# Optimization experiments

Hardware: AMD Instinct MI355X
Metric: run time of the kernel (lower is better)

Reference implementation:

```python
import jax, jax.numpy as jnp
import numpy as np

B, S, HID, H, DK = 2, 2048, 1024, 16, 64
SCALE = DK ** -0.5
NEG = -1000000000.0


def setup_inputs() -> dict:
    key = jax.random.key(0)
    ks = jax.random.split(key, 14)
    std = HID ** -0.5
    return {
        "q": jax.random.normal(ks[0], (B, S, HID), jnp.float32),
        "k": jax.random.normal(ks[1], (B, S, HID), jnp.float32),
        "v": jax.random.normal(ks[2], (B, S, HID), jnp.float32),
        "attn_bias": jax.random.normal(ks[3], (B, H, S, S), jnp.float32),
        "mask": jax.random.randint(ks[4], (B, S), 0, 2, jnp.int32),
        "Wq": jax.random.normal(ks[5], (HID, H * DK), jnp.float32) * std,
        "bq": jnp.zeros((H * DK,), jnp.float32),
        "Wk": jax.random.normal(ks[6], (HID, H * DK), jnp.float32) * std,
        "bk": jnp.zeros((H * DK,), jnp.float32),
        "Wv": jax.random.normal(ks[7], (HID, H * DK), jnp.float32) * std,
        "bv": jnp.zeros((H * DK,), jnp.float32),
        "Wo": jax.random.normal(ks[8], (H * DK, H * DK), jnp.float32) * std,
        "bo": jnp.zeros((H * DK,), jnp.float32),
    }


def reference(q, k, v, attn_bias, mask, Wq, bq, Wk, bk, Wv, bv, Wo, bo):
    Bq = q.shape[0]
    # projections -> [B, H, S, DK]
    qh = (q @ Wq + bq).reshape(Bq, -1, H, DK).transpose(0, 2, 1, 3) * SCALE
    kh = (k @ Wk + bk).reshape(Bq, -1, H, DK).transpose(0, 2, 1, 3)
    vh = (v @ Wv + bv).reshape(Bq, -1, H, DK).transpose(0, 2, 1, 3)
    # scores [B, H, Sq, Sk]
    scores = jnp.einsum("bhqd,bhkd->bhqk", qh, kh)
    k_mask = mask[:, None, None, :]  # [B,1,1,Sk]
    scores = jnp.where(k_mask == 0, NEG, scores)
    scores = scores + attn_bias
    attn = jax.nn.softmax(scores, axis=-1)  # dropout rate 0.0 -> identity
    x = jnp.einsum("bhqk,bhkd->bhqd", attn, vh)
    x = x * mask[:, None, :, None].astype(x.dtype)  # zero masked query rows
    x = x.transpose(0, 2, 1, 3).reshape(Bq, -1, H * DK)
    return x @ Wo + bo
```

## Files before the change

### kernel.cpp

```cpp
#include <hip/hip_runtime.h>


typedef __bf16 bf16x8 __attribute__((ext_vector_type(8)));
typedef float f32x4 __attribute__((ext_vector_type(4)));
typedef unsigned short u16x8 __attribute__((ext_vector_type(8)));

#define NEGV (-1000000000.0f)

typedef __attribute__((address_space(3))) unsigned int lds_u32;
typedef const __attribute__((address_space(1))) unsigned int glb_u32;

static __device__ __forceinline__ void async16(const void* g, void* l) {
  __builtin_amdgcn_global_load_lds((glb_u32*)g, (lds_u32*)l, 16, 0, 0);
}

static __device__ __forceinline__ unsigned short f2b(float f) {
  unsigned int u = __float_as_uint(f);
  return (unsigned short)((u + 0x7FFFu + ((u >> 16) & 1u)) >> 16);
}

static __device__ __forceinline__ bf16x8 ld8(const unsigned short* p) {
  return __builtin_bit_cast(bf16x8, *(const u16x8*)p);
}

__global__ __launch_bounds__(256) void k_wtrans(const float* __restrict__ W0, const float* __restrict__ W1,
                                                const float* __restrict__ W2, const float* __restrict__ W3,
                                                unsigned short* __restrict__ T0, unsigned short* __restrict__ T1,
                                                unsigned short* __restrict__ T2, unsigned short* __restrict__ T3) {
  const float* W = (blockIdx.z == 0) ? W0 : (blockIdx.z == 1) ? W1 : (blockIdx.z == 2) ? W2 : W3;
  unsigned short* Wt = (blockIdx.z == 0) ? T0 : (blockIdx.z == 1) ? T1 : (blockIdx.z == 2) ? T2 : T3;
  __shared__ float tile[32][33];
  int k0 = blockIdx.x * 32, n0 = blockIdx.y * 32;
  int tx = threadIdx.x, ty = threadIdx.y;
  #pragma unroll
  for (int i = 0; i < 32; i += 8)
    tile[ty + i][tx] = W[(size_t)(k0 + ty + i) * 1024 + n0 + tx];
  __syncthreads();
  #pragma unroll
  for (int i = 0; i < 32; i += 8)
    Wt[(size_t)(n0 + ty + i) * 1024 + k0 + tx] = f2b(tile[tx][ty + i]);
}

__global__ __launch_bounds__(256) void k_gemm(const float* __restrict__ Af,
                                              const unsigned short* __restrict__ Ab,
                                              const unsigned short* __restrict__ Bt,
                                              const float* __restrict__ bias,
                                              unsigned short* __restrict__ outb,
                                              float* __restrict__ outf, int mode) {
  __shared__ __align__(16) unsigned short smem[128 * 136];
  unsigned short* As = smem;
  unsigned short* Bs = smem + 128 * 64;
  int t = threadIdx.x;
  int wave = t >> 6, lane = t & 63;
  int r16 = lane & 15, quad = lane >> 4, quad8 = quad * 8;
  int wm = (wave >> 1) * 64, wn = (wave & 1) * 64;
  int n0 = blockIdx.x * 128, m0 = blockIdx.y * 128;
  f32x4 acc[4][4] = {};

  for (int k0 = 0; k0 < 1024; k0 += 64) {
    __syncthreads();
    if (mode != 3) {
      int g = t & 7;
      #pragma unroll
      for (int rr = 0; rr < 4; rr++) {
        int row = (t >> 3) + rr * 32;
        const float* p = Af + (size_t)(m0 + row) * 1024 + k0 + g * 8;
        float4 f0 = *(const float4*)p;
        float4 f1 = *(const float4*)(p + 4);
        u16x8 h;
        h[0] = f2b(f0.x); h[1] = f2b(f0.y); h[2] = f2b(f0.z); h[3] = f2b(f0.w);
        h[4] = f2b(f1.x); h[5] = f2b(f1.y); h[6] = f2b(f1.z); h[7] = f2b(f1.w);
        *(u16x8*)&As[row * 64 + ((g ^ (row & 7))) * 8] = h;
      }
    } else {
      #pragma unroll
      for (int i = 0; i < 4; i++) {
        int row = wave * 32 + i * 8 + (lane >> 3);
        const unsigned short* g = Ab + (size_t)(m0 + row) * 1024 + k0 + (((lane & 7) ^ (row & 7))) * 8;
        async16(g, &As[(wave * 32 + i * 8) * 64]);
      }
    }
    #pragma unroll
    for (int i = 0; i < 4; i++) {
      int row = wave * 32 + i * 8 + (lane >> 3);
      const unsigned short* g = Bt + (size_t)(n0 + row) * 1024 + k0 + (((lane & 7) ^ (row & 7))) * 8;
      async16(g, &Bs[(wave * 32 + i * 8) * 64]);
    }
    __syncthreads();
    #pragma unroll
    for (int kk2 = 0; kk2 < 2; kk2++) {
      bf16x8 av[4], bv[4];
      int gq = quad + kk2 * 4;
      #pragma unroll
      for (int mt = 0; mt < 4; mt++) {
        int lm = wm + mt * 16 + r16;
        av[mt] = ld8(&As[lm * 64 + (gq ^ (lm & 7)) * 8]);
      }
      #pragma unroll
      for (int nt = 0; nt < 4; nt++) {
        int ln = wn + nt * 16 + r16;
        bv[nt] = ld8(&Bs[ln * 64 + (gq ^ (ln & 7)) * 8]);
      }
      #pragma unroll
      for (int mt = 0; mt < 4; mt++)
        #pragma unroll
        for (int nt = 0; nt < 4; nt++)
          acc[mt][nt] = __builtin_amdgcn_mfma_f32_16x16x32_bf16(av[mt], bv[nt], acc[mt][nt], 0, 0, 0);
    }
  }

  if (mode == 3) {
    #pragma unroll
    for (int nt = 0; nt < 4; nt++) {
      int gn = n0 + wn + nt * 16 + r16;
      float bv = bias[gn];
      #pragma unroll
      for (int mt = 0; mt < 4; mt++)
        #pragma unroll
        for (int r = 0; r < 4; r++) {
          int gm = m0 + wm + mt * 16 + quad * 4 + r;
          outf[(size_t)gm * 1024 + gn] = acc[mt][nt][r] + bv;
        }
    }
    return;
  }

  __syncthreads();
  float scale = (mode == 0) ? 0.125f : 1.0f;
  #pragma unroll
  for (int nt = 0; nt < 4; nt++) {
    int ln = wn + nt * 16 + r16;
    float bv = bias[n0 + ln];
    #pragma unroll
    for (int mt = 0; mt < 4; mt++)
      #pragma unroll
      for (int r = 0; r < 4; r++) {
        int lm = wm + mt * 16 + quad * 4 + r;
        unsigned short hv = f2b((acc[mt][nt][r] + bv) * scale);
        if (mode == 2) smem[ln * 136 + lm] = hv;
        else           smem[lm * 136 + ln] = hv;
      }
  }
  __syncthreads();
  int rrow = t >> 1, half = t & 1;
  const unsigned short* src = smem + rrow * 136 + half * 64;
  if (mode == 2) {
    int b = m0 >> 11, s0 = m0 & 2047;
    int gn = n0 + rrow, h = gn >> 6, d = gn & 63;
    unsigned short* dst = outb + ((size_t)(b * 16 + h) * 64 + d) * 2048 + s0 + half * 64;
    #pragma unroll
    for (int j = 0; j < 8; j++) *(int4*)(dst + j * 8) = *(const int4*)(src + j * 8);
  } else {
    int gm = m0 + rrow, b = gm >> 11, s = gm & 2047;
    int h = (n0 + half * 64) >> 6;
    unsigned short* dst = outb + ((size_t)(b * 16 + h) * 2048 + s) * 64;
    #pragma unroll
    for (int j = 0; j < 8; j++) *(int4*)(dst + j * 8) = *(const int4*)(src + j * 8);
  }
}

__global__ __launch_bounds__(256) void k_attn(const unsigned short* __restrict__ qh,
                                              const unsigned short* __restrict__ kh,
                                              const unsigned short* __restrict__ vt,
                                              const float* __restrict__ bias,
                                              const int* __restrict__ mask,
                                              unsigned short* __restrict__ xb) {
  __shared__ __align__(16) unsigned short Ks[64 * 72];
  __shared__ __align__(16) unsigned short Vs[64 * 72];
  __shared__ __align__(16) unsigned short Ps[64 * 72];
  __shared__ float kmb[64];
  int t = threadIdx.x;
  int wave = t >> 6, lane = t & 63;
  int r16 = lane & 15, quad = lane >> 4, quad8 = quad * 8;
  int w16 = wave * 16;
  int q0 = blockIdx.x * 64;
  int bh = blockIdx.y;
  int b = bh >> 4, h = bh & 15;
  const unsigned short* kbase = kh + (size_t)bh * 2048 * 64;
  const unsigned short* vbase = vt + (size_t)bh * 64 * 2048;
  const float* bbase = bias + (size_t)bh * 2048 * 2048 + (size_t)q0 * 2048;

  bf16x8 qf[2];
  {
    const unsigned short* qrow = qh + (size_t)bh * 2048 * 64 + (size_t)(q0 + w16 + r16) * 64;
    qf[0] = ld8(qrow + quad8);
    qf[1] = ld8(qrow + 32 + quad8);
  }
  const u16x8 onesu = {0x3F80, 0x3F80, 0x3F80, 0x3F80, 0x3F80, 0x3F80, 0x3F80, 0x3F80};
  const bf16x8 ones = __builtin_bit_cast(bf16x8, onesu);

  f32x4 o[4] = {};
  f32x4 accl = {};
  float mrow[4] = {-1e38f, -1e38f, -1e38f, -1e38f};

  for (int k0 = 0; k0 < 2048; k0 += 64) {
    __syncthreads();
    {
      int row = t >> 2, c = (t & 3) * 16;
      *(int4*)&Ks[row * 72 + c]     = *(const int4*)(kbase + (size_t)(k0 + row) * 64 + c);
      *(int4*)&Ks[row * 72 + c + 8] = *(const int4*)(kbase + (size_t)(k0 + row) * 64 + c + 8);
      *(int4*)&Vs[row * 72 + c]     = *(const int4*)(vbase + (size_t)row * 2048 + k0 + c);
      *(int4*)&Vs[row * 72 + c + 8] = *(const int4*)(vbase + (size_t)row * 2048 + k0 + c + 8);
    }
    if (t < 64) kmb[t] = (mask[b * 2048 + k0 + t] == 0) ? 1.0f : 0.0f;
    __syncthreads();

    f32x4 sc[4] = {};
    #pragma unroll
    for (int kk2 = 0; kk2 < 2; kk2++) {
      #pragma unroll
      for (int nt = 0; nt < 4; nt++) {
        bf16x8 bb = ld8(&Ks[(nt * 16 + r16) * 72 + kk2 * 32 + quad8]);
        sc[nt] = __builtin_amdgcn_mfma_f32_16x16x32_bf16(qf[kk2], bb, sc[nt], 0, 0, 0);
      }
    }
    #pragma unroll
    for (int nt = 0; nt < 4; nt++) {
      float km = kmb[nt * 16 + r16];
      #pragma unroll
      for (int r = 0; r < 4; r++) {
        float bval = bbase[(size_t)(w16 + quad * 4 + r) * 2048 + k0 + nt * 16 + r16];
        sc[nt][r] = ((km > 0.5f) ? NEGV : sc[nt][r]) + bval;
      }
    }
    float arow[4];
    #pragma unroll
    for (int r = 0; r < 4; r++) {
      float mx = fmaxf(fmaxf(sc[0][r], sc[1][r]), fmaxf(sc[2][r], sc[3][r]));
      #pragma unroll
      for (int off = 1; off < 16; off <<= 1) mx = fmaxf(mx, __shfl_xor(mx, off));
      float mn = fmaxf(mrow[r], mx);
      arow[r] = __expf(mrow[r] - mn);
      mrow[r] = mn;
      #pragma unroll
      for (int nt = 0; nt < 4; nt++) sc[nt][r] = __expf(sc[nt][r] - mn);
    }
    #pragma unroll
    for (int nt = 0; nt < 4; nt++)
      #pragma unroll
      for (int r = 0; r < 4; r++)
        Ps[(w16 + quad * 4 + r) * 72 + nt * 16 + r16] = f2b(sc[nt][r]);
    #pragma unroll
    for (int r = 0; r < 4; r++) {
      accl[r] *= arow[r];
      #pragma unroll
      for (int nt = 0; nt < 4; nt++) o[nt][r] *= arow[r];
    }
    #pragma unroll
    for (int kk2 = 0; kk2 < 2; kk2++) {
      bf16x8 a = ld8(&Ps[(w16 + r16) * 72 + kk2 * 32 + quad8]);
      accl = __builtin_amdgcn_mfma_f32_16x16x32_bf16(a, ones, accl, 0, 0, 0);
      #pragma unroll
      for (int nt = 0; nt < 4; nt++) {
        bf16x8 bb = ld8(&Vs[(nt * 16 + r16) * 72 + kk2 * 32 + quad8]);
        o[nt] = __builtin_amdgcn_mfma_f32_16x16x32_bf16(a, bb, o[nt], 0, 0, 0);
      }
    }
  }

  float inv[4];
  #pragma unroll
  for (int r = 0; r < 4; r++) {
    int gq = q0 + w16 + quad * 4 + r;
    float qm = (mask[b * 2048 + gq] != 0) ? 1.0f : 0.0f;
    inv[r] = qm / accl[r];
  }
  #pragma unroll
  for (int nt = 0; nt < 4; nt++)
    #pragma unroll
    for (int r = 0; r < 4; r++) {
      int gq = q0 + w16 + quad * 4 + r;
      xb[(size_t)(b * 2048 + gq) * 1024 + h * 64 + nt * 16 + r16] = f2b(o[nt][r] * inv[r]);
    }
}

extern "C" void kernel_launch(void* const* d_in, const int* in_sizes, int n_in,
                              void* d_out, int out_size, void* d_ws, size_t ws_size,
                              hipStream_t stream) {
  const float* q = (const float*)d_in[0];
  const float* k = (const float*)d_in[1];
  const float* v = (const float*)d_in[2];
  const float* attn_bias = (const float*)d_in[3];
  const int* mask = (const int*)d_in[4];
  const float* Wq = (const float*)d_in[5];
  const float* bq = (const float*)d_in[6];
  const float* Wk = (const float*)d_in[7];
  const float* bk = (const float*)d_in[8];
  const float* Wv = (const float*)d_in[9];
  const float* bv = (const float*)d_in[10];
  const float* Wo = (const float*)d_in[11];
  const float* bo = (const float*)d_in[12];

  char* ws = (char*)d_ws;
  const size_t MB = 1u << 20;
  unsigned short* Wqt = (unsigned short*)(ws + 0 * MB);
  unsigned short* Wkt = (unsigned short*)(ws + 2 * MB);
  unsigned short* Wvt = (unsigned short*)(ws + 4 * MB);
  unsigned short* Wot = (unsigned short*)(ws + 6 * MB);
  unsigned short* qhb = (unsigned short*)(ws + 8 * MB);
  unsigned short* khb = (unsigned short*)(ws + 16 * MB);
  unsigned short* vtb = (unsigned short*)(ws + 24 * MB);
  unsigned short* xbb = (unsigned short*)(ws + 32 * MB);

  k_wtrans<<<dim3(32, 32, 4), dim3(32, 8), 0, stream>>>(Wq, Wk, Wv, Wo, Wqt, Wkt, Wvt, Wot);

  dim3 gg(8, 32), gb(256);
  k_gemm<<<gg, gb, 0, stream>>>(q, nullptr, Wqt, bq, qhb, nullptr, 0);
  k_gemm<<<gg, gb, 0, stream>>>(k, nullptr, Wkt, bk, khb, nullptr, 1);
  k_gemm<<<gg, gb, 0, stream>>>(v, nullptr, Wvt, bv, vtb, nullptr, 2);

  k_attn<<<dim3(32, 32), 256, 0, stream>>>(qhb, khb, vtb, attn_bias, mask, xbb);

  k_gemm<<<gg, gb, 0, stream>>>(nullptr, xbb, Wot, bo, nullptr, (float*)d_out, 3);
}
```

Baseline: 927.9 us.

## Batch QKV GEMMs, add 64x64 output GEMM, widen attention tile to 128 queries

The three projection GEMMs become one launch that picks its operands from blockIdx.z, which cuts launch overhead and fills more CUs at once. The output projection moves to its own kernel with 64x64 tiles, giving four times as many blocks for better occupancy. The attention kernel now handles 128 query rows per block (32 per wave), so each K/V tile loaded is reused twice as much. K/V are loaded asynchronously into swizzled LDS instead of padded tiles. Per-wave register use roughly doubles in attention, and the attention grid halves to 512 blocks.

Result: faster. 885.4 us (-4.6%).

```diff
diff --git a/kernel.cpp b/kernel.cpp
--- a/kernel.cpp
+++ b/kernel.cpp
@@ -41,25 +41,31 @@
     Wt[(size_t)(n0 + ty + i) * 1024 + k0 + tx] = f2b(tile[tx][ty + i]);
 }
 
-__global__ __launch_bounds__(256) void k_gemm(const float* __restrict__ Af,
-                                              const unsigned short* __restrict__ Ab,
-                                              const unsigned short* __restrict__ Bt,
-                                              const float* __restrict__ bias,
-                                              unsigned short* __restrict__ outb,
-                                              float* __restrict__ outf, int mode) {
+__global__ __launch_bounds__(256) void k_gemm_qkv(
+    const float* __restrict__ A0, const float* __restrict__ A1, const float* __restrict__ A2,
+    const unsigned short* __restrict__ W0, const unsigned short* __restrict__ W1,
+    const unsigned short* __restrict__ W2,
+    const float* __restrict__ b0, const float* __restrict__ b1, const float* __restrict__ b2,
+    unsigned short* __restrict__ o0, unsigned short* __restrict__ o1, unsigned short* __restrict__ o2) {
+  int mode = blockIdx.z;
+  const float* Af = (mode == 0) ? A0 : (mode == 1) ? A1 : A2;
+  const unsigned short* Bt = (mode == 0) ? W0 : (mode == 1) ? W1 : W2;
+  const float* bias = (mode == 0) ? b0 : (mode == 1) ? b1 : b2;
+  unsigned short* outb = (mode == 0) ? o0 : (mode == 1) ? o1 : o2;
+
   __shared__ __align__(16) unsigned short smem[128 * 136];
   unsigned short* As = smem;
   unsigned short* Bs = smem + 128 * 64;
   int t = threadIdx.x;
   int wave = t >> 6, lane = t & 63;
-  int r16 = lane & 15, quad = lane >> 4, quad8 = quad * 8;
+  int r16 = lane & 15, quad = lane >> 4;
   int wm = (wave >> 1) * 64, wn = (wave & 1) * 64;
   int n0 = blockIdx.x * 128, m0 = blockIdx.y * 128;
   f32x4 acc[4][4] = {};
 
   for (int k0 = 0; k0 < 1024; k0 += 64) {
     __syncthreads();
-    if (mode != 3) {
+    {
       int g = t & 7;
       #pragma unroll
       for (int rr = 0; rr < 4; rr++) {
@@ -72,13 +78,6 @@
         h[4] = f2b(f1.x); h[5] = f2b(f1.y); h[6] = f2b(f1.z); h[7] = f2b(f1.w);
         *(u16x8*)&As[row * 64 + ((g ^ (row & 7))) * 8] = h;
       }
-    } else {
-      #pragma unroll
-      for (int i = 0; i < 4; i++) {
-        int row = wave * 32 + i * 8 + (lane >> 3);
-        const unsigned short* g = Ab + (size_t)(m0 + row) * 1024 + k0 + (((lane & 7) ^ (row & 7))) * 8;
-        async16(g, &As[(wave * 32 + i * 8) * 64]);
-      }
     }
     #pragma unroll
     for (int i = 0; i < 4; i++) {
@@ -107,22 +106,6 @@
         for (int nt = 0; nt < 4; nt++)
           acc[mt][nt] = __builtin_amdgcn_mfma_f32_16x16x32_bf16(av[mt], bv[nt], acc[mt][nt], 0, 0, 0);
     }
-  }
-
-  if (mode == 3) {
-    #pragma unroll
-    for (int nt = 0; nt < 4; nt++) {
-      int gn = n0 + wn + nt * 16 + r16;
-      float bv = bias[gn];
-      #pragma unroll
-      for (int mt = 0; mt < 4; mt++)
-        #pragma unroll
-        for (int r = 0; r < 4; r++) {
-          int gm = m0 + wm + mt * 16 + quad * 4 + r;
-          outf[(size_t)gm * 1024 + gn] = acc[mt][nt][r] + bv;
-        }
-    }
-    return;
   }
 
   __syncthreads();
@@ -159,119 +142,195 @@
   }
 }
 
+__global__ __launch_bounds__(256) void k_gemm_o(const unsigned short* __restrict__ Ab,
+                                                const unsigned short* __restrict__ Bt,
+                                                const float* __restrict__ bias,
+                                                float* __restrict__ outf) {
+  __shared__ __align__(16) unsigned short As[64 * 64];
+  __shared__ __align__(16) unsigned short Bs[64 * 64];
+  int t = threadIdx.x;
+  int wave = t >> 6, lane = t & 63;
+  int r16 = lane & 15, quad = lane >> 4;
+  int w16 = wave * 16;
+  int n0 = blockIdx.x * 64, m0 = blockIdx.y * 64;
+  f32x4 acc[4] = {};
+
+  for (int k0 = 0; k0 < 1024; k0 += 64) {
+    __syncthreads();
+    #pragma unroll
+    for (int i = 0; i < 2; i++) {
+      int row = wave * 16 + i * 8 + (lane >> 3);
+      const unsigned short* ga = Ab + (size_t)(m0 + row) * 1024 + k0 + (((lane & 7) ^ (row & 7))) * 8;
+      async16(ga, &As[(wave * 16 + i * 8) * 64]);
+      const unsigned short* gb = Bt + (size_t)(n0 + row) * 1024 + k0 + (((lane & 7) ^ (row & 7))) * 8;
+      async16(gb, &Bs[(wave * 16 + i * 8) * 64]);
+    }
+    __syncthreads();
+    #pragma unroll
+    for (int kk2 = 0; kk2 < 2; kk2++) {
+      int gq = quad + kk2 * 4;
+      int lm = w16 + r16;
+      bf16x8 a = ld8(&As[lm * 64 + (gq ^ (lm & 7)) * 8]);
+      #pragma unroll
+      for (int nt = 0; nt < 4; nt++) {
+        int ln = nt * 16 + r16;
+        bf16x8 bb = ld8(&Bs[ln * 64 + (gq ^ (ln & 7)) * 8]);
+        acc[nt] = __builtin_amdgcn_mfma_f32_16x16x32_bf16(a, bb, acc[nt], 0, 0, 0);
+      }
+    }
+  }
+  #pragma unroll
+  for (int nt = 0; nt < 4; nt++) {
+    int gn = n0 + nt * 16 + r16;
+    float bv = bias[gn];
+    #pragma unroll
+    for (int r = 0; r < 4; r++) {
+      int gm = m0 + w16 + quad * 4 + r;
+      outf[(size_t)gm * 1024 + gn] = acc[nt][r] + bv;
+    }
+  }
+}
+
 __global__ __launch_bounds__(256) void k_attn(const unsigned short* __restrict__ qh,
                                               const unsigned short* __restrict__ kh,
                                               const unsigned short* __restrict__ vt,
                                               const float* __restrict__ bias,
                                               const int* __restrict__ mask,
                                               unsigned short* __restrict__ xb) {
-  __shared__ __align__(16) unsigned short Ks[64 * 72];
-  __shared__ __align__(16) unsigned short Vs[64 * 72];
-  __shared__ __align__(16) unsigned short Ps[64 * 72];
+  __shared__ __align__(16) unsigned short Ks[64 * 64];
+  __shared__ __align__(16) unsigned short Vs[64 * 64];
+  __shared__ __align__(16) unsigned short Ps[128 * 72];
   __shared__ float kmb[64];
   int t = threadIdx.x;
   int wave = t >> 6, lane = t & 63;
   int r16 = lane & 15, quad = lane >> 4, quad8 = quad * 8;
-  int w16 = wave * 16;
-  int q0 = blockIdx.x * 64;
+  int w32 = wave * 32;
+  int q0 = blockIdx.x * 128;
   int bh = blockIdx.y;
   int b = bh >> 4, h = bh & 15;
   const unsigned short* kbase = kh + (size_t)bh * 2048 * 64;
   const unsigned short* vbase = vt + (size_t)bh * 64 * 2048;
   const float* bbase = bias + (size_t)bh * 2048 * 2048 + (size_t)q0 * 2048;
 
-  bf16x8 qf[2];
-  {
-    const unsigned short* qrow = qh + (size_t)bh * 2048 * 64 + (size_t)(q0 + w16 + r16) * 64;
-    qf[0] = ld8(qrow + quad8);
-    qf[1] = ld8(qrow + 32 + quad8);
+  bf16x8 qf[2][2];
+  #pragma unroll
+  for (int mt = 0; mt < 2; mt++) {
+    const unsigned short* qrow = qh + (size_t)bh * 2048 * 64 + (size_t)(q0 + w32 + mt * 16 + r16) * 64;
+    qf[mt][0] = ld8(qrow + quad8);
+    qf[mt][1] = ld8(qrow + 32 + quad8);
   }
   const u16x8 onesu = {0x3F80, 0x3F80, 0x3F80, 0x3F80, 0x3F80, 0x3F80, 0x3F80, 0x3F80};
   const bf16x8 ones = __builtin_bit_cast(bf16x8, onesu);
 
-  f32x4 o[4] = {};
-  f32x4 accl = {};
-  float mrow[4] = {-1e38f, -1e38f, -1e38f, -1e38f};
+  f32x4 o[2][4] = {};
+  f32x4 accl[2] = {};
+  float mrow[2][4] = {{-1e38f, -1e38f, -1e38f, -1e38f}, {-1e38f, -1e38f, -1e38f, -1e38f}};
 
   for (int k0 = 0; k0 < 2048; k0 += 64) {
     __syncthreads();
-    {
-      int row = t >> 2, c = (t & 3) * 16;
-      *(int4*)&Ks[row * 72 + c]     = *(const int4*)(kbase + (size_t)(k0 + row) * 64 + c);
-      *(int4*)&Ks[row * 72 + c + 8] = *(const int4*)(kbase + (size_t)(k0 + row) * 64 + c + 8);
-      *(int4*)&Vs[row * 72 + c]     = *(const int4*)(vbase + (size_t)row * 2048 + k0 + c);
-      *(int4*)&Vs[row * 72 + c + 8] = *(const int4*)(vbase + (size_t)row * 2048 + k0 + c + 8);
+    #pragma unroll
+    for (int j = 0; j < 2; j++) {
+      int row = wave * 16 + j * 8 + (lane >> 3);
+      int sw = (((lane & 7) ^ (row & 7))) * 8;
+      async16(kbase + (size_t)(k0 + row) * 64 + sw, &Ks[(wave * 16 + j * 8) * 64]);
+      async16(vbase + (size_t)row * 2048 + k0 + sw, &Vs[(wave * 16 + j * 8) * 64]);
     }
     if (t < 64) kmb[t] = (mask[b * 2048 + k0 + t] == 0) ? 1.0f : 0.0f;
     __syncthreads();
 
-    f32x4 sc[4] = {};
+    f32x4 sc[2][4] = {};
     #pragma unroll
     for (int kk2 = 0; kk2 < 2; kk2++) {
-      #pragma unroll
-      for (int nt = 0; nt < 4; nt++) {
-        bf16x8 bb = ld8(&Ks[(nt * 16 + r16) * 72 + kk2 * 32 + quad8]);
-        sc[nt] = __builtin_amdgcn_mfma_f32_16x16x32_bf16(qf[kk2], bb, sc[nt], 0, 0, 0);
-      }
-    }
-    #pragma unroll
-    for (int nt = 0; nt < 4; nt++) {
-      float km = kmb[nt * 16 + r16];
+      bf16x8 kf[4];
+      int gq = quad + kk2 * 4;
+      #pragma unroll
+      for (int nt = 0; nt < 4; nt++) {
+        int ln = nt * 16 + r16;
+        kf[nt] = ld8(&Ks[ln * 64 + (gq ^ (ln & 7)) * 8]);
+      }
+      #pragma unroll
+      for (int mt = 0; mt < 2; mt++)
+        #pragma unroll
+        for (int nt = 0; nt < 4; nt++)
+          sc[mt][nt] = __builtin_amdgcn_mfma_f32_16x16x32_bf16(qf[mt][kk2], kf[nt], sc[mt][nt], 0, 0, 0);
+    }
+    #pragma unroll
+    for (int mt = 0; mt < 2; mt++)
+      #pragma unroll
+      for (int nt = 0; nt < 4; nt++) {
+        float km = kmb[nt * 16 + r16];
+        #pragma unroll
+        for (int r = 0; r < 4; r++) {
+          float bval = bbase[(size_t)(w32 + mt * 16 + quad * 4 + r) * 2048 + k0 + nt * 16 + r16];
+          sc[mt][nt][r] = ((km > 0.5f) ? NEGV : sc[mt][nt][r]) + bval;
+        }
+      }
+    float arow[2][4];
+    #pragma unroll
+    for (int mt = 0; mt < 2; mt++)
       #pragma unroll
       for (int r = 0; r < 4; r++) {
-        float bval = bbase[(size_t)(w16 + quad * 4 + r) * 2048 + k0 + nt * 16 + r16];
-        sc[nt][r] = ((km > 0.5f) ? NEGV : sc[nt][r]) + bval;
-      }
-    }
-    float arow[4];
+        float mx = fmaxf(fmaxf(sc[mt][0][r], sc[mt][1][r]), fmaxf(sc[mt][2][r], sc[mt][3][r]));
+        #pragma unroll
+        for (int off = 1; off < 16; off <<= 1) mx = fmaxf(mx, __shfl_xor(mx, off));
+        float mn = fmaxf(mrow[mt][r], mx);
+        arow[mt][r] = __expf(mrow[mt][r] - mn);
+        mrow[mt][r] = mn;
+        #pragma unroll
+        for (int nt = 0; nt < 4; nt++) sc[mt][nt][r] = __expf(sc[mt][nt][r] - mn);
+      }
+    #pragma unroll
+    for (int mt = 0; mt < 2; mt++)
+      #pragma unroll
+      for (int nt = 0; nt < 4; nt++)
+        #pragma unroll
+        for (int r = 0; r < 4; r++)
+          Ps[(w32 + mt * 16 + quad * 4 + r) * 72 + nt * 16 + r16] = f2b(sc[mt][nt][r]);
+    #pragma unroll
+    for (int mt = 0; mt < 2; mt++)
+      #pragma unroll
+      for (int r = 0; r < 4; r++) {
+        accl[mt][r] *= arow[mt][r];
+        #pragma unroll
+        for (int nt = 0; nt < 4; nt++) o[mt][nt][r] *= arow[mt][r];
+      }
+    #pragma unroll
+    for (int kk2 = 0; kk2 < 2; kk2++) {
+      bf16x8 vf[4];
+      int gq = quad + kk2 * 4;
+      #pragma unroll
+      for (int nt = 0; nt < 4; nt++) {
+        int ln = nt * 16 + r16;
+        vf[nt] = ld8(&Vs[ln * 64 + (gq ^ (ln & 7)) * 8]);
+      }
+      #pragma unroll
+      for (int mt = 0; mt < 2; mt++) {
+        bf16x8 a = ld8(&Ps[(w32 + mt * 16 + r16) * 72 + kk2 * 32 + quad8]);
+        accl[mt] = __builtin_amdgcn_mfma_f32_16x16x32_bf16(a, ones, accl[mt], 0, 0, 0);
+        #pragma unroll
+        for (int nt = 0; nt < 4; nt++)
+          o[mt][nt] = __builtin_amdgcn_mfma_f32_16x16x32_bf16(a, vf[nt], o[mt][nt], 0, 0, 0);
+      }
+    }
+  }
+
+  #pragma unroll
+  for (int mt = 0; mt < 2; mt++) {
+    float inv[4];
     #pragma unroll
     for (int r = 0; r < 4; r++) {
-      float mx = fmaxf(fmaxf(sc[0][r], sc[1][r]), fmaxf(sc[2][r], sc[3][r]));
-      #pragma unroll
-      for (int off = 1; off < 16; off <<= 1) mx = fmaxf(mx, __shfl_xor(mx, off));
-      float mn = fmaxf(mrow[r], mx);
-      arow[r] = __expf(mrow[r] - mn);
-      mrow[r] = mn;
-      #pragma unroll
-      for (int nt = 0; nt < 4; nt++) sc[nt][r] = __expf(sc[nt][r] - mn);
+      int gq = q0 + w32 + mt * 16 + quad * 4 + r;
+      float qm = (mask[b * 2048 + gq] != 0) ? 1.0f : 0.0f;
+      inv[r] = qm / accl[mt][r];
     }
     #pragma unroll
     for (int nt = 0; nt < 4; nt++)
       #pragma unroll
-      for (int r = 0; r < 4; r++)
-        Ps[(w16 + quad * 4 + r) * 72 + nt * 16 + r16] = f2b(sc[nt][r]);
-    #pragma unroll
-    for (int r = 0; r < 4; r++) {
-      accl[r] *= arow[r];
-      #pragma unroll
-      for (int nt = 0; nt < 4; nt++) o[nt][r] *= arow[r];
-    }
-    #pragma unroll
-    for (int kk2 = 0; kk2 < 2; kk2++) {
-      bf16x8 a = ld8(&Ps[(w16 + r16) * 72 + kk2 * 32 + quad8]);
-      accl = __builtin_amdgcn_mfma_f32_16x16x32_bf16(a, ones, accl, 0, 0, 0);
-      #pragma unroll
-      for (int nt = 0; nt < 4; nt++) {
-        bf16x8 bb = ld8(&Vs[(nt * 16 + r16) * 72 + kk2 * 32 + quad8]);
-        o[nt] = __builtin_amdgcn_mfma_f32_16x16x32_bf16(a, bb, o[nt], 0, 0, 0);
-      }
-    }
-  }
-
-  float inv[4];
-  #pragma unroll
-  for (int r = 0; r < 4; r++) {
-    int gq = q0 + w16 + quad * 4 + r;
-    float qm = (mask[b * 2048 + gq] != 0) ? 1.0f : 0.0f;
-    inv[r] = qm / accl[r];
-  }
-  #pragma unroll
-  for (int nt = 0; nt < 4; nt++)
-    #pragma unroll
-    for (int r = 0; r < 4; r++) {
-      int gq = q0 + w16 + quad * 4 + r;
-      xb[(size_t)(b * 2048 + gq) * 1024 + h * 64 + nt * 16 + r16] = f2b(o[nt][r] * inv[r]);
-    }
+      for (int r = 0; r < 4; r++) {
+        int gq = q0 + w32 + mt * 16 + quad * 4 + r;
+        xb[(size_t)(b * 2048 + gq) * 1024 + h * 64 + nt * 16 + r16] = f2b(o[mt][nt][r] * inv[r]);
+      }
+  }
 }
 
 extern "C" void kernel_launch(void* const* d_in, const int* in_sizes, int n_in,
@@ -304,12 +363,10 @@
 
   k_wtrans<<<dim3(32, 32, 4), dim3(32, 8), 0, stream>>>(Wq, Wk, Wv, Wo, Wqt, Wkt, Wvt, Wot);
 
-  dim3 gg(8, 32), gb(256);
-  k_gemm<<<gg, gb, 0, stream>>>(q, nullptr, Wqt, bq, qhb, nullptr, 0);
-  k_gemm<<<gg, gb, 0, stream>>>(k, nullptr, Wkt, bk, khb, nullptr, 1);
-  k_gemm<<<gg, gb, 0, stream>>>(v, nullptr, Wvt, bv, vtb, nullptr, 2);
-
-  k_attn<<<dim3(32, 32), 256, 0, stream>>>(qhb, khb, vtb, attn_bias, mask, xbb);
-
-  k_gemm<<<gg, gb, 0, stream>>>(nullptr, xbb, Wot, bo, nullptr, (float*)d_out, 3);
-}
+  k_gemm_qkv<<<dim3(8, 32, 3), 256, 0, stream>>>(q, k, v, Wqt, Wkt, Wvt, bq, bk, bv,
+                                                 qhb, khb, vtb);
+
+  k_attn<<<dim3(16, 32), 256, 0, stream>>>(qhb, khb, vtb, attn_bias, mask, xbb);
+
+  k_gemm_o<<<dim3(16, 64), 256, 0, stream>>>(xbb, Wot, bo, (float*)d_out);
+}
```
